# Optimization experiments

Hardware: AMD Instinct MI355X
Metric: run time of the kernel (lower is better)

Reference implementation:

```python
import jax, jax.numpy as jnp
import numpy as np

EPS = 1e-05
NEG = -1000000000.0

def rmsnorm(x):
    var = jnp.mean(x * x, axis=-1, keepdims=True)
    return x * jax.lax.rsqrt(var + EPS)

def apply_rotary(x, cos, sin):
    # x: [B,T,H,D], cos/sin: [T,D]
    d = x.shape[-1]
    x1, x2 = x[..., : d // 2], x[..., d // 2 :]
    half_rot = jnp.concatenate([-x2, x1], axis=-1)
    c = cos[None, :, None, :]
    s = sin[None, :, None, :]
    return x * c + half_rot * s

def setup_inputs() -> dict:
    key = jax.random.key(0)
    ks = jax.random.split(key, 12)
    B, T, C, H = 2, 2048, 1024, 16
    hd = C // H
    std = 0.02
    return {
        "x": jax.random.normal(ks[0], (B, T, C), jnp.float32),
        "x0": jax.random.normal(ks[1], (B, T, C), jnp.float32),
        "lambdaResid": jnp.ones((), jnp.float32),
        "lambdaX0": jnp.ones((), jnp.float32),
        "cos": jax.random.uniform(ks[2], (T, hd), jnp.float32),
        "sin": jax.random.uniform(ks[3], (T, hd), jnp.float32),
        "qWeight": jax.random.normal(ks[4], (C, C), jnp.float32) * std,
        "kWeight": jax.random.normal(ks[5], (C, C), jnp.float32) * std,
        "vWeight": jax.random.normal(ks[6], (C, C), jnp.float32) * std,
        "projWeight": jax.random.normal(ks[7], (C, C), jnp.float32) * std,
        "fcWeight": jax.random.normal(ks[8], (C, 4 * C), jnp.float32) * std,
        "mlpProjWeight": jax.random.normal(ks[9], (4 * C, C), jnp.float32) * std,
    }

def reference(x, x0, lambdaResid, lambdaX0, cos, sin,
              qWeight, kWeight, vWeight, projWeight, fcWeight, mlpProjWeight):
    B, T, C = x.shape
    hd = cos.shape[-1]
    H = C // hd
    scaled = x * lambdaResid + x0 * lambdaX0
    pre = rmsnorm(scaled)
    q = (pre @ qWeight).reshape(B, T, H, hd)
    k = (pre @ kWeight).reshape(B, T, H, hd)
    v = (pre @ vWeight).reshape(B, T, H, hd)
    q = rmsnorm(apply_rotary(q, cos, sin))  # [B,T,H,D]
    k = rmsnorm(apply_rotary(k, cos, sin))
    scores = jnp.einsum('bthd,bshd->bhts', q, k) / jnp.sqrt(jnp.float32(hd))
    mask = jnp.tril(jnp.ones((T, T), bool))
    scores = jnp.where(mask[None, None], scores, NEG)
    probs = jax.nn.softmax(scores, axis=-1)
    attn = jnp.einsum('bhts,bshd->bthd', probs, v).reshape(B, T, C)
    scaled = scaled + attn @ projWeight
    h = rmsnorm(scaled) @ fcWeight
    h = jnp.square(jax.nn.relu(h))
    return scaled + h @ mlpProjWeight
```

## Files before the change

### kernel.cpp

```cpp
#include <hip/hip_runtime.h>
#include <hip/hip_bf16.h>
#include <stdint.h>

typedef _Float16 f16;
typedef __attribute__((ext_vector_type(8))) _Float16 f16x8;
typedef __attribute__((ext_vector_type(4))) _Float16 f16x4;
typedef __attribute__((ext_vector_type(2))) __fp16 fp16x2;
typedef __attribute__((ext_vector_type(4))) float f32x4;

__device__ __forceinline__ void g2l16(const void* g, void* l) {
  __builtin_amdgcn_global_load_lds(
      (const __attribute__((address_space(1))) uint32_t*)g,
      (__attribute__((address_space(3))) uint32_t*)l, 16, 0, 0);
}

__device__ __forceinline__ uint32_t pkrtz(float a, float b) {
  union { fp16x2 h; uint32_t u; } z;
  z.h = __builtin_amdgcn_cvt_pkrtz(a, b);
  return z.u;
}

__global__ __launch_bounds__(256)
void wconv_all_kernel(const float* __restrict__ Wq, const float* __restrict__ Wk,
                      const float* __restrict__ Wv, const float* __restrict__ Wp,
                      const float* __restrict__ Wfc, const float* __restrict__ Wmp,
                      f16* __restrict__ Dq, f16* __restrict__ Dk, f16* __restrict__ Dv,
                      f16* __restrict__ Dp, f16* __restrict__ Dfc, f16* __restrict__ Dmp)
{
  __shared__ float tile[32][33];
  int id = blockIdx.x;
  const float* W; f16* Wt; int K, N, local;
  if      (id < 1024) { W = Wq;  Wt = Dq;  K = 1024; N = 1024; local = id; }
  else if (id < 2048) { W = Wk;  Wt = Dk;  K = 1024; N = 1024; local = id - 1024; }
  else if (id < 3072) { W = Wv;  Wt = Dv;  K = 1024; N = 1024; local = id - 2048; }
  else if (id < 4096) { W = Wp;  Wt = Dp;  K = 1024; N = 1024; local = id - 3072; }
  else if (id < 8192) { W = Wfc; Wt = Dfc; K = 1024; N = 4096; local = id - 4096; }
  else                { W = Wmp; Wt = Dmp; K = 4096; N = 1024; local = id - 8192; }
  int ntx = N >> 5;
  int n0 = (local % ntx) * 32, k0 = (local / ntx) * 32;
  int tx = threadIdx.x & 31, ty = threadIdx.x >> 5;
#pragma unroll
  for (int i = 0; i < 4; ++i)
    tile[ty + 8*i][tx] = W[(size_t)(k0 + ty + 8*i) * N + (n0 + tx)];
  __syncthreads();
#pragma unroll
  for (int i = 0; i < 4; ++i)
    Wt[(size_t)(n0 + ty + 8*i) * K + (k0 + tx)] = (f16)tile[tx][ty + 8*i];
}

__global__ __launch_bounds__(256)
void scale_rms_kernel(const float* __restrict__ x, const float* __restrict__ x0,
                      const float* __restrict__ lamR, const float* __restrict__ lamX,
                      float* __restrict__ scaled, f16* __restrict__ pre)
{
  const int C = 1024;
  int row = blockIdx.x, tid = threadIdx.x;
  float lr = lamR[0], lx = lamX[0];
  size_t base = (size_t)row * C;
  float4 xv = ((const float4*)(x + base))[tid];
  float4 zv = ((const float4*)(x0 + base))[tid];
  float4 sv;
  sv.x = xv.x*lr + zv.x*lx;  sv.y = xv.y*lr + zv.y*lx;
  sv.z = xv.z*lr + zv.z*lx;  sv.w = xv.w*lr + zv.w*lx;
  float ss = sv.x*sv.x + sv.y*sv.y + sv.z*sv.z + sv.w*sv.w;
#pragma unroll
  for (int off = 32; off >= 1; off >>= 1) ss += __shfl_xor(ss, off);
  __shared__ float red[4];
  if ((tid & 63) == 0) red[tid >> 6] = ss;
  __syncthreads();
  float tot = red[0] + red[1] + red[2] + red[3];
  float rs = rsqrtf(tot * (1.0f / 1024.0f) + 1e-5f);
  ((float4*)(scaled + base))[tid] = sv;
  f16* p = pre + base + tid * 4;
  p[0] = (f16)(sv.x * rs); p[1] = (f16)(sv.y * rs);
  p[2] = (f16)(sv.z * rs); p[3] = (f16)(sv.w * rs);
}

__global__ __launch_bounds__(256)
void combine_rms_kernel(const float* __restrict__ resid, const f16* __restrict__ p0,
                        const f16* __restrict__ p1, float* __restrict__ scaled2,
                        f16* __restrict__ pre2)
{
  const int C = 1024;
  int row = blockIdx.x, tid = threadIdx.x;
  size_t base = (size_t)row * C;
  float4 rv = ((const float4*)(resid + base))[tid];
  f16x4 av = ((const f16x4*)(p0 + base))[tid];
  f16x4 bv = ((const f16x4*)(p1 + base))[tid];
  float4 sv;
  sv.x = rv.x + (float)av[0] + (float)bv[0];
  sv.y = rv.y + (float)av[1] + (float)bv[1];
  sv.z = rv.z + (float)av[2] + (float)bv[2];
  sv.w = rv.w + (float)av[3] + (float)bv[3];
  float ss = sv.x*sv.x + sv.y*sv.y + sv.z*sv.z + sv.w*sv.w;
#pragma unroll
  for (int off = 32; off >= 1; off >>= 1) ss += __shfl_xor(ss, off);
  __shared__ float red[4];
  if ((tid & 63) == 0) red[tid >> 6] = ss;
  __syncthreads();
  float tot = red[0] + red[1] + red[2] + red[3];
  float rs = rsqrtf(tot * (1.0f / 1024.0f) + 1e-5f);
  ((float4*)(scaled2 + base))[tid] = sv;
  f16* p = pre2 + base + tid * 4;
  p[0] = (f16)(sv.x * rs); p[1] = (f16)(sv.y * rs);
  p[2] = (f16)(sv.z * rs); p[3] = (f16)(sv.w * rs);
}

__global__ __launch_bounds__(256)
void combine_out4_kernel(const float* __restrict__ resid, const f16* __restrict__ parts,
                         size_t pstride, float* __restrict__ out)
{
  size_t i = (size_t)blockIdx.x * 256 + threadIdx.x;
  float4 rv = ((const float4*)resid)[i];
  float4 sv = rv;
#pragma unroll
  for (int z = 0; z < 4; ++z) {
    f16x4 av = ((const f16x4*)(parts + z * pstride))[i];
    sv.x += (float)av[0]; sv.y += (float)av[1];
    sv.z += (float)av[2]; sv.w += (float)av[3];
  }
  ((float4*)out)[i] = sv;
}

__global__ __launch_bounds__(256)
void rope_rms_kernel(f16* __restrict__ Xq, f16* __restrict__ Xk,
                     const float* __restrict__ cs, const float* __restrict__ sn)
{
  const int MH = 4096 * 16;
  int ridx = blockIdx.x * 4 + (threadIdx.x >> 6);
  f16* X = (ridx < MH) ? Xq : Xk;
  if (ridx >= MH) ridx -= MH;
  int lane = threadIdx.x & 63;
  int h = ridx & 15;
  int bt = ridx >> 4;
  int t = bt & 2047;
  size_t base = (size_t)bt * 1024 + h * 64;
  float xv = (float)X[base + lane];
  float other = __shfl_xor(xv, 32);
  float rot = (lane < 32) ? -other : other;
  float c = cs[t * 64 + lane], s = sn[t * 64 + lane];
  float y = xv * c + rot * s;
  float ss = y * y;
#pragma unroll
  for (int off = 32; off >= 1; off >>= 1) ss += __shfl_xor(ss, off);
  float r = rsqrtf(ss * (1.0f / 64.0f) + 1e-5f);
  X[base + lane] = (f16)(y * r);
}

template<int EPI>
__global__ __launch_bounds__(256)
void gemm_kernel(const f16* __restrict__ A, const f16* __restrict__ Bt,
                 void* __restrict__ out, int M, int N, int K, int nb, int zb)
{
  __shared__ __align__(16) f16 smem[4 * 128 * 32];
  const int tid = threadIdx.x;
  const int wave = tid >> 6, lane = tid & 63;
  const int col = lane & 15, quad = lane >> 4;
  const int id = blockIdx.x;
  const int xcd = id & 7, s = id >> 3;
  const int n_i = s % nb;
  const int p = s / nb;
  const int mpx = (M >> 7) >> 3;
  const int zz = p / mpx;
  const int m_i = xcd * mpx + (p % mpx);
  const int m0 = m_i * 128, n0 = n_i * 128;
  const int wm = (wave >> 1) * 64, wn = (wave & 1) * 64;
  const int Ksub = K / zb;
  const int kBeg = zz * Ksub;
  const int nIter = Ksub >> 5;
  f32x4 acc[4][4] = {};

  const size_t rowb = (size_t)K * 2;
  const char* Agp = (const char*)A  + (size_t)m0 * rowb;
  const char* Bgp = (const char*)Bt + (size_t)n0 * rowb;

  const int r_st = (tid >> 2);
  const int cb_st = (tid & 3) << 4;
  const int lb0 = (wave * 64) << 4;
  const int lb1 = (256 + wave * 64) << 4;

#define STAGE(buf, k0)                                                           \
  {                                                                              \
    const size_t koff = (size_t)(k0) * 2;                                        \
    g2l16(Agp + (size_t)r_st * rowb + koff + cb_st,                              \
          (char*)smem + (buf) * 8192 + lb0);                                     \
    g2l16(Agp + (size_t)(r_st + 64) * rowb + koff + cb_st,                       \
          (char*)smem + (buf) * 8192 + lb1);                                     \
    g2l16(Bgp + (size_t)r_st * rowb + koff + cb_st,                              \
          (char*)smem + 16384 + (buf) * 8192 + lb0);                             \
    g2l16(Bgp + (size_t)(r_st + 64) * rowb + koff + cb_st,                       \
          (char*)smem + 16384 + (buf) * 8192 + lb1);                             \
  }

  STAGE(0, kBeg)
  for (int kt = 0; kt < nIter; ++kt) {
    __syncthreads();
    if (kt + 1 < nIter) STAGE((kt + 1) & 1, kBeg + (kt + 1) * 32)
    const f16* As = smem + (kt & 1) * 4096;
    const f16* Bs = smem + 8192 + (kt & 1) * 4096;
    f16x8 af[4], bf[4];
#pragma unroll
    for (int t = 0; t < 4; ++t)
      af[t] = *(const f16x8*)(As + (wm + t*16 + col) * 32 + quad * 8);
#pragma unroll
    for (int t = 0; t < 4; ++t)
      bf[t] = *(const f16x8*)(Bs + (wn + t*16 + col) * 32 + quad * 8);
#pragma unroll
    for (int mt = 0; mt < 4; ++mt)
#pragma unroll
      for (int nt = 0; nt < 4; ++nt)
        acc[mt][nt] = __builtin_amdgcn_mfma_f32_16x16x32_f16(af[mt], bf[nt], acc[mt][nt], 0, 0, 0);
  }
#undef STAGE
  f16* ep = smem + wave * 1024;
  f16* outz = (EPI == 4) ? ((f16*)out + (size_t)zz * M * N) : (f16*)out;
#pragma unroll
  for (int mt = 0; mt < 4; ++mt) {
#pragma unroll
    for (int nt = 0; nt < 4; ++nt) {
#pragma unroll
      for (int r = 0; r < 4; ++r) {
        float v = acc[mt][nt][r];
        if (EPI == 1) { float tv = v > 0.0f ? v : 0.0f; v = tv * tv; }
        ep[(quad * 4 + r) * 64 + ((nt ^ quad) * 16 + col)] = (f16)v;
      }
    }
#pragma unroll
    for (int j = 0; j < 2; ++j) {
      int e = j * 64 + lane;
      int row = e >> 3, rb = e & 7;
      int phys16 = (((rb >> 1) ^ (row >> 2)) << 1) + (rb & 1);
      f16x8 vv = *(const f16x8*)(ep + row * 64 + phys16 * 8);
      int grow = m0 + wm + mt * 16 + row;
      int gcol = n0 + wn + rb * 8;
      *(f16x8*)(outz + (size_t)grow * N + gcol) = vv;
    }
  }
}

__device__ __forceinline__ void stage256(const char* Agp, const char* Bgp, size_t rowb,
                                         char* lds, int st_r, size_t koff, int tid)
{
#pragma unroll
  for (int j = 0; j < 4; ++j) {
    g2l16(Agp + (size_t)(st_r + j * 64) * rowb + koff, lds + j * 8192 + tid * 16);
    g2l16(Bgp + (size_t)(st_r + j * 64) * rowb + koff, lds + 32768 + j * 8192 + tid * 16);
  }
}

template<int EPI>
__global__ __launch_bounds__(512, 2)
void gemm256_kernel(const f16* __restrict__ A, const f16* __restrict__ Bt,
                    void* __restrict__ out, int M, int N, int K, int nb, int zb)
{
  __shared__ __align__(16) f16 smem[65536];
  const int tid = threadIdx.x;
  const int wave = tid >> 6, lane = tid & 63;
  const int col = lane & 15, quad = lane >> 4;
  const int id = blockIdx.x;
  const int xcd = id & 7, sb = id >> 3;
  const int n_i = sb % nb;
  const int p = sb / nb;
  const int mpx = (M >> 8) >> 3;
  const int zz = p / mpx;
  const int m_i = xcd * mpx + (p % mpx);
  const int m0 = m_i * 256, n0 = n_i * 256;
  const int wm = (wave >> 2) * 128, wn = (wave & 3) * 64;
  const int Ksub = K / zb;
  const int kBeg = zz * Ksub;
  const int ntiles = Ksub >> 6;
  f32x4 acc[8][4] = {};

  const size_t rowb = (size_t)K * 2;
  const char* Agp = (const char*)A  + (size_t)m0 * rowb;
  const char* Bgp = (const char*)Bt + (size_t)n0 * rowb;

  const int st_r = tid >> 3;
  const size_t st_so = (size_t)(((tid & 7) ^ ((tid >> 3) & 7)) << 4);

  stage256(Agp, Bgp, rowb, (char*)smem,         st_r, (size_t)kBeg * 2 + st_so, tid);
  stage256(Agp, Bgp, rowb, (char*)smem + 65536, st_r, (size_t)(kBeg + 64) * 2 + st_so, tid);

  for (int t = 0; t < ntiles; ++t) {
    if (t < ntiles - 1) asm volatile("s_waitcnt vmcnt(8)" ::: "memory");
    else                asm volatile("s_waitcnt vmcnt(0)" ::: "memory");
    __builtin_amdgcn_s_barrier();
    asm volatile("" ::: "memory");

    const f16* As = smem + (t & 1) * 32768;
    const f16* Bs = As + 16384;
    f16x8 bf[4][2];
#pragma unroll
    for (int ct = 0; ct < 4; ++ct)
#pragma unroll
      for (int ks = 0; ks < 2; ++ks)
        bf[ct][ks] = *(const f16x8*)(Bs + (wn + ct*16 + col) * 64 +
                                     (((ks*4 + quad) ^ (col & 7)) << 3));
#pragma unroll
    for (int sp = 0; sp < 4; ++sp) {
      f16x8 af[2][2];
#pragma unroll
      for (int i = 0; i < 2; ++i)
#pragma unroll
        for (int ks = 0; ks < 2; ++ks)
          af[i][ks] = *(const f16x8*)(As + (wm + (sp*2 + i)*16 + col) * 64 +
                                      (((ks*4 + quad) ^ (col & 7)) << 3));
      __builtin_amdgcn_s_setprio(1);
#pragma unroll
      for (int i = 0; i < 2; ++i)
#pragma unroll
        for (int ct = 0; ct < 4; ++ct)
#pragma unroll
          for (int ks = 0; ks < 2; ++ks)
            acc[sp*2 + i][ct] = __builtin_amdgcn_mfma_f32_16x16x32_f16(
                af[i][ks], bf[ct][ks], acc[sp*2 + i][ct], 0, 0, 0);
      __builtin_amdgcn_s_setprio(0);
    }

    asm volatile("s_waitcnt lgkmcnt(0)" ::: "memory");
    __builtin_amdgcn_s_barrier();
    asm volatile("" ::: "memory");
    if (t + 2 < ntiles)
      stage256(Agp, Bgp, rowb, (char*)smem + (t & 1) * 65536, st_r,
               (size_t)(kBeg + (t + 2) * 64) * 2 + st_so, tid);
  }

  f16* ep = smem + wave * 1024;
  f16* outz = (EPI == 4) ? ((f16*)out + (size_t)zz * M * N) : (f16*)out;
#pragma unroll
  for (int mt = 0; mt < 8; ++mt) {
#pragma unroll
    for (int ct = 0; ct < 4; ++ct) {
#pragma unroll
      for (int r = 0; r < 4; ++r) {
        float v = acc[mt][ct][r];
        if (EPI == 1) { float tv = v > 0.0f ? v : 0.0f; v = tv * tv; }
        ep[(quad * 4 + r) * 64 + ((ct ^ quad) * 16 + col)] = (f16)v;
      }
    }
#pragma unroll
    for (int j = 0; j < 2; ++j) {
      int e = j * 64 + lane;
      int row = e >> 3, rb = e & 7;
      int phys16 = (((rb >> 1) ^ (row >> 2)) << 1) + (rb & 1);
      f16x8 vv = *(const f16x8*)(ep + row * 64 + phys16 * 8);
      int grow = m0 + wm + mt * 16 + row;
      int gcol = n0 + wn + rb * 8;
      *(f16x8*)(outz + (size_t)grow * N + gcol) = vv;
    }
  }
}

__global__ __launch_bounds__(512, 2)
void gemm256_qkv_kernel(const f16* __restrict__ A, const f16* __restrict__ Bt,
                        f16* __restrict__ qb, f16* __restrict__ kbuf, f16* __restrict__ vtg)
{
  const int K = 1024, nb = 12, ntiles = 16;
  __shared__ __align__(16) f16 smem[65536];
  const int tid = threadIdx.x;
  const int wave = tid >> 6, lane = tid & 63;
  const int col = lane & 15, quad = lane >> 4;
  const int id = blockIdx.x;
  const int xcd = id & 7, sb = id >> 3;
  const int n_i = sb % nb;
  const int m_i = xcd * 2 + (sb / nb);
  const int m0 = m_i * 256, n0 = n_i * 256;
  const int wm = (wave >> 2) * 128, wn = (wave & 3) * 64;
  f32x4 acc[8][4] = {};

  const size_t rowb = (size_t)K * 2;
  const char* Agp = (const char*)A  + (size_t)m0 * rowb;
  const char* Bgp = (const char*)Bt + (size_t)n0 * rowb;

  const int st_r = tid >> 3;
  const size_t st_so = (size_t)(((tid & 7) ^ ((tid >> 3) & 7)) << 4);

  stage256(Agp, Bgp, rowb, (char*)smem,         st_r, st_so, tid);
  stage256(Agp, Bgp, rowb, (char*)smem + 65536, st_r, (size_t)64 * 2 + st_so, tid);

  for (int t = 0; t < ntiles; ++t) {
    if (t < ntiles - 1) asm volatile("s_waitcnt vmcnt(8)" ::: "memory");
    else                asm volatile("s_waitcnt vmcnt(0)" ::: "memory");
    __builtin_amdgcn_s_barrier();
    asm volatile("" ::: "memory");

    const f16* As = smem + (t & 1) * 32768;
    const f16* Bs = As + 16384;
    f16x8 bf[4][2];
#pragma unroll
    for (int ct = 0; ct < 4; ++ct)
#pragma unroll
      for (int ks = 0; ks < 2; ++ks)
        bf[ct][ks] = *(const f16x8*)(Bs + (wn + ct*16 + col) * 64 +
                                     (((ks*4 + quad) ^ (col & 7)) << 3));
#pragma unroll
    for (int sp = 0; sp < 4; ++sp) {
      f16x8 af[2][2];
#pragma unroll
      for (int i = 0; i < 2; ++i)
#pragma unroll
        for (int ks = 0; ks < 2; ++ks)
          af[i][ks] = *(const f16x8*)(As + (wm + (sp*2 + i)*16 + col) * 64 +
                                      (((ks*4 + quad) ^ (col & 7)) << 3));
      __builtin_amdgcn_s_setprio(1);
#pragma unroll
      for (int i = 0; i < 2; ++i)
#pragma unroll
        for (int ct = 0; ct < 4; ++ct)
#pragma unroll
          for (int ks = 0; ks < 2; ++ks)
            acc[sp*2 + i][ct] = __builtin_amdgcn_mfma_f32_16x16x32_f16(
                af[i][ks], bf[ct][ks], acc[sp*2 + i][ct], 0, 0, 0);
      __builtin_amdgcn_s_setprio(0);
    }

    asm volatile("s_waitcnt lgkmcnt(0)" ::: "memory");
    __builtin_amdgcn_s_barrier();
    asm volatile("" ::: "memory");
    if (t + 2 < ntiles)
      stage256(Agp, Bgp, rowb, (char*)smem + (t & 1) * 65536, st_r,
               (size_t)((t + 2) * 64) * 2 + st_so, tid);
  }

  const int cw = n0 + wn;
  const int sel = cw >> 10;
  if (sel < 2) {
    f16* dst = (sel == 0) ? qb : kbuf;
    const int cbase = cw & 1023;
    f16* ep = smem + wave * 1024;
#pragma unroll
    for (int mt = 0; mt < 8; ++mt) {
#pragma unroll
      for (int ct = 0; ct < 4; ++ct)
#pragma unroll
        for (int r = 0; r < 4; ++r)
          ep[(quad * 4 + r) * 64 + ((ct ^ quad) * 16 + col)] = (f16)acc[mt][ct][r];
#pragma unroll
      for (int j = 0; j < 2; ++j) {
        int e = j * 64 + lane;
        int row = e >> 3, rb = e & 7;
        int phys16 = (((rb >> 1) ^ (row >> 2)) << 1) + (rb & 1);
        f16x8 vv = *(const f16x8*)(ep + row * 64 + phys16 * 8);
        int grow = m0 + wm + mt * 16 + row;
        *(f16x8*)(dst + (size_t)grow * 1024 + cbase + rb * 8) = vv;
      }
    }
  } else {
#pragma unroll
    for (int mt = 0; mt < 8; ++mt) {
      int t0 = m0 + wm + mt * 16 + quad * 4;
      int b = t0 >> 11, t = t0 & 2047;
#pragma unroll
      for (int ct = 0; ct < 4; ++ct) {
        int dd = (cw & 1023) + ct * 16 + col;
        int hh = dd >> 6, d = dd & 63;
        f16x4 vv;
#pragma unroll
        for (int r = 0; r < 4; ++r) vv[r] = (f16)acc[mt][ct][r];
        *(f16x4*)(vtg + ((size_t)((b * 16 + hh) * 64 + d)) * 2048 + t) = vv;
      }
    }
  }
}

__global__ __launch_bounds__(256, 5)
void attn_kernel(const f16* __restrict__ Q, const f16* __restrict__ Kc,
                 const f16* __restrict__ Vt, f16* __restrict__ O,
                 f16* __restrict__ pO, float* __restrict__ pL)
{
  const int T = 2048, C = 1024;
  __shared__ __align__(16) f16 Ks[2][64 * 64];
  __shared__ __align__(16) f16 Vs[2][64 * 64];
  const int tid = threadIdx.x, wave = tid >> 6, lane = tid & 63;
  const int col = lane & 15, quad = lane >> 4;
  const int bh = blockIdx.x, b = bh >> 4, h = bh & 15;

  const int u = blockIdx.y;
  int qt = 0, acc0 = 0, nc = 1;
  for (int q = 0; q < 32; ++q) {
    int c = (q + 8) >> 3;
    if (u < acc0 + c) { qt = q; nc = c; break; }
    acc0 += c;
  }
  const int ci = u - acc0;
  const int n = qt + 1;
  const int kt0 = (ci * n) / nc, kt1 = ((ci + 1) * n) / nc;
  const int q0 = qt * 64;

  const f16* qb = Q  + ((size_t)b * T) * C + h * 64;
  const f16* kb = Kc + ((size_t)b * T) * C + h * 64;
  const f16* vb = Vt + ((size_t)bh * 64) * T;

  f16x8 bq[2];
#pragma unroll
  for (int ks = 0; ks < 2; ++ks)
    bq[ks] = *(const f16x8*)(qb + (size_t)(q0 + wave*16 + col) * C + ks*32 + quad*8);

  f32x4 o_acc[4];
#pragma unroll
  for (int dt = 0; dt < 4; ++dt) o_acc[dt] = (f32x4){0.f,0.f,0.f,0.f};
  float l_acc = 0.f;

  const int srow = lane >> 3;
  const int sblk = (lane & 7) ^ srow;

#pragma unroll
  for (int i = 0; i < 2; ++i) {
    int r0 = wave * 16 + 8 * i;
    g2l16(kb + (size_t)(kt0 * 64 + r0 + srow) * C + sblk * 8, (char*)Ks[0] + r0 * 128);
    g2l16(vb + (size_t)(r0 + srow) * T + kt0 * 64 + sblk * 8, (char*)Vs[0] + r0 * 128);
  }

  const int cm = col & 7;
  const int c00 = quad,            c01 = 4 + (quad ^ 1);
  const int c10 = 8 + (quad ^ 2),  c11 = 12 + (quad ^ 3);
  const int o00 = (((c00 >> 1) ^ cm) << 3) + ((c00 & 1) << 2);
  const int o01 = (((c01 >> 1) ^ cm) << 3) + ((c01 & 1) << 2);
  const int o10 = (((c10 >> 1) ^ cm) << 3) + ((c10 & 1) << 2);
  const int o11 = (((c11 >> 1) ^ cm) << 3) + ((c11 & 1) << 2);

  int cur = 0;
  for (int kt = kt0; kt < kt1; ++kt) {
    __syncthreads();

    if (kt + 1 < kt1) {
      const int ks1 = (kt + 1) * 64;
#pragma unroll
      for (int i = 0; i < 2; ++i) {
        int r0 = wave * 16 + 8 * i;
        g2l16(kb + (size_t)(ks1 + r0 + srow) * C + sblk * 8, (char*)Ks[cur ^ 1] + r0 * 128);
        g2l16(vb + (size_t)(r0 + srow) * T + ks1 + sblk * 8, (char*)Vs[cur ^ 1] + r0 * 128);
      }
    }

    f32x4 s[4];
#pragma unroll
    for (int nt = 0; nt < 4; ++nt) s[nt] = (f32x4){0.f,0.f,0.f,0.f};
    __builtin_amdgcn_s_setprio(1);
#pragma unroll
    for (int ks = 0; ks < 2; ++ks) {
#pragma unroll
      for (int nt = 0; nt < 4; ++nt) {
        int key = nt * 16 + col;
        f16x8 ak = *(const f16x8*)(Ks[cur] + key * 64 + (((ks*4 + quad) ^ (key & 7)) * 8));
        s[nt] = __builtin_amdgcn_mfma_f32_16x16x32_f16(ak, bq[ks], s[nt], 0, 0, 0);
      }
    }
    __builtin_amdgcn_s_setprio(0);

    const bool masked = (kt == qt);
    const int qloc = wave * 16 + col;
    uint32_t pk[4][2];
    float l_tile = 0.f;
#pragma unroll
    for (int nt = 0; nt < 4; ++nt) {
      float p[4];
#pragma unroll
      for (int r = 0; r < 4; ++r) {
        float pv = __expf(s[nt][r] * 0.125f);
        if (masked && (nt * 16 + quad * 4 + r > qloc)) pv = 0.0f;
        p[r] = pv;
      }
      l_tile += (p[0] + p[1]) + (p[2] + p[3]);
      pk[nt][0] = pkrtz(p[0], p[1]);
      pk[nt][1] = pkrtz(p[2], p[3]);
    }
    l_acc += l_tile;

    union { uint32_t u[4]; f16x8 v; } pa0, pa1;
    pa0.u[0] = pk[0][0];
    pa0.u[1] = pk[0][1];
    pa0.u[2] = (uint32_t)__shfl_xor((int)pk[1][0], 16);
    pa0.u[3] = (uint32_t)__shfl_xor((int)pk[1][1], 16);
    pa1.u[0] = (uint32_t)__shfl_xor((int)pk[2][0], 32);
    pa1.u[1] = (uint32_t)__shfl_xor((int)pk[2][1], 32);
    pa1.u[2] = (uint32_t)__shfl_xor((int)pk[3][0], 48);
    pa1.u[3] = (uint32_t)__shfl_xor((int)pk[3][1], 48);

    __builtin_amdgcn_s_setprio(1);
#pragma unroll
    for (int dt = 0; dt < 4; ++dt) {
      const f16* vrow = Vs[cur] + (dt * 16 + col) * 64;
      union { struct { f16x4 lo, hi; } p; f16x8 v; } bv0, bv1;
      bv0.p.lo = *(const f16x4*)(vrow + o00);
      bv0.p.hi = *(const f16x4*)(vrow + o01);
      bv1.p.lo = *(const f16x4*)(vrow + o10);
      bv1.p.hi = *(const f16x4*)(vrow + o11);
      o_acc[dt] = __builtin_amdgcn_mfma_f32_16x16x32_f16(pa0.v, bv0.v, o_acc[dt], 0, 0, 0);
      o_acc[dt] = __builtin_amdgcn_mfma_f32_16x16x32_f16(pa1.v, bv1.v, o_acc[dt], 0, 0, 0);
    }
    __builtin_amdgcn_s_setprio(0);
    cur ^= 1;
  }

  l_acc += __shfl_xor(l_acc, 16);
  l_acc += __shfl_xor(l_acc, 32);

  if (nc == 1) {
    float linv[4];
#pragma unroll
    for (int r = 0; r < 4; ++r)
      linv[r] = 1.0f / __shfl(l_acc, quad * 4 + r);
#pragma unroll
    for (int dt = 0; dt < 4; ++dt) {
#pragma unroll
      for (int r = 0; r < 4; ++r) {
        int qr = q0 + wave * 16 + quad * 4 + r;
        float v = o_acc[dt][r] * linv[r];
        O[((size_t)b * T + qr) * C + h * 64 + dt * 16 + col] = (f16)v;
      }
    }
  } else {
    const size_t slot = (size_t)bh * 80 + u;
    f16* po = pO + slot * 4096;
#pragma unroll
    for (int dt = 0; dt < 4; ++dt)
#pragma unroll
      for (int r = 0; r < 4; ++r)
        po[(wave * 16 + quad * 4 + r) * 64 + dt * 16 + col] = (f16)o_acc[dt][r];
    if (quad == 0) pL[slot * 64 + wave * 16 + col] = l_acc;
  }
}

__global__ __launch_bounds__(256)
void attn_combine_kernel(const f16* __restrict__ pO, const float* __restrict__ pL,
                         f16* __restrict__ O)
{
  const int T = 2048, C = 1024;
  const int bh = blockIdx.x, b = bh >> 4, h = bh & 15;
  const int qt = 8 + blockIdx.y;
  const int nc = (qt + 8) >> 3;
  int pre = 0;
  for (int q = 0; q < qt; ++q) pre += (q + 8) >> 3;
  const size_t slot0 = (size_t)bh * 80 + pre;

  const int t = threadIdx.x;
  const int row = t >> 2, dq = (t & 3) * 16;

  float L = 0.f;
  for (int ci = 0; ci < nc; ++ci) L += pL[(slot0 + ci) * 64 + row];
  const float inv = 1.0f / L;

  float acc[16] = {};
  for (int ci = 0; ci < nc; ++ci) {
    const f16x8* p = (const f16x8*)(pO + (slot0 + ci) * 4096 + row * 64 + dq);
    f16x8 v0 = p[0], v1 = p[1];
#pragma unroll
    for (int j = 0; j < 8; ++j) { acc[j] += (float)v0[j]; acc[8 + j] += (float)v1[j]; }
  }
  f16x8 o0, o1;
#pragma unroll
  for (int j = 0; j < 8; ++j) { o0[j] = (f16)(acc[j] * inv); o1[j] = (f16)(acc[8 + j] * inv); }
  f16* dst = O + ((size_t)b * T + qt * 64 + row) * C + h * 64 + dq;
  ((f16x8*)dst)[0] = o0;
  ((f16x8*)dst)[1] = o1;
}

extern "C" void kernel_launch(void* const* d_in, const int* in_sizes, int n_in,
                              void* d_out, int out_size, void* d_ws, size_t ws_size,
                              hipStream_t stream)
{
  const float* x    = (const float*)d_in[0];
  const float* x0   = (const float*)d_in[1];
  const float* lamR = (const float*)d_in[2];
  const float* lamX = (const float*)d_in[3];
  const float* cs   = (const float*)d_in[4];
  const float* sn   = (const float*)d_in[5];
  const float* Wq   = (const float*)d_in[6];
  const float* Wk   = (const float*)d_in[7];
  const float* Wv   = (const float*)d_in[8];
  const float* Wp   = (const float*)d_in[9];
  const float* Wfc  = (const float*)d_in[10];
  const float* Wmp  = (const float*)d_in[11];
  float* out = (float*)d_out;

  const int B = 2, T = 2048, C = 1024, H = 16;
  const int M = B * T;
  const size_t MB = 1ull << 20;
  char* ws = (char*)d_ws;
  f16*   Wqkv_t = (f16*)(ws + 0 * MB);
  f16*   Wp_t   = (f16*)(ws + 6 * MB);
  f16*   Wfc_t  = (f16*)(ws + 8 * MB);
  f16*   Wmp_t  = (f16*)(ws + 16 * MB);
  float* scaled  = (float*)(ws + 24 * MB);
  f16*   pre     = (f16*)(ws + 40 * MB);
  f16*   qb      = (f16*)(ws + 48 * MB);
  f16*   kbuf    = (f16*)(ws + 56 * MB);
  f16*   vtg     = (f16*)(ws + 64 * MB);
  float* scaled2 = (float*)(ws + 72 * MB);
  f16*   hbuf    = (f16*)(ws + 88 * MB);
  f16*   attnOut = pre;
  f16*   pre2    = qb;
  f16*   projP   = (f16*)(ws + 88 * MB);
  f16*   mlpP    = (f16*)(ws + 24 * MB);
  f16*   attnPO  = (f16*)(ws + 88 * MB);
  float* attnPL  = (float*)(ws + 108 * MB);

  dim3 tb(256);
  dim3 tb5(512);
  wconv_all_kernel<<<dim3(12288), tb, 0, stream>>>(
      Wq, Wk, Wv, Wp, Wfc, Wmp,
      Wqkv_t, Wqkv_t + 1024*1024, Wqkv_t + 2048*1024, Wp_t, Wfc_t, Wmp_t);

  scale_rms_kernel<<<M, tb, 0, stream>>>(x, x0, lamR, lamX, scaled, pre);

  gemm256_qkv_kernel<<<dim3(192), tb5, 0, stream>>>(pre, Wqkv_t, qb, kbuf, vtg);

  rope_rms_kernel<<<(M * H) / 2, tb, 0, stream>>>(qb, kbuf, cs, sn);

  attn_kernel<<<dim3(B * H, 80), tb, 0, stream>>>(qb, kbuf, vtg, attnOut, attnPO, attnPL);
  attn_combine_kernel<<<dim3(B * H, 24), tb, 0, stream>>>(attnPO, attnPL, attnOut);

  gemm_kernel<4><<<dim3(8 * 32 * 2), tb, 0, stream>>>(attnOut, Wp_t, projP, M, C, C, 8, 2);
  combine_rms_kernel<<<M, tb, 0, stream>>>(scaled, projP, projP + (size_t)M*C, scaled2, pre2);

  gemm256_kernel<1><<<dim3(256), tb5, 0, stream>>>(pre2, Wfc_t, hbuf, M, 4*C, C, 16, 1);

  gemm256_kernel<4><<<dim3(256), tb5, 0, stream>>>(hbuf, Wmp_t, mlpP, M, C, 4*C, 4, 4);
  combine_out4_kernel<<<(M*C)/1024, tb, 0, stream>>>(scaled2, mlpP, (size_t)M*C, out);
}
```

Before: 351.8 us.

## Prefetch K/V two tiles ahead with partial vmcnt waits in attention

The attention loop now issues the async global-to-LDS loads for tile kt+2 right after tile kt is consumed, and starts with two tiles in flight. At the top of each iteration it waits only until the current tile's loads land (vmcnt(4)) rather than draining all loads with a full __syncthreads. This deepens the load pipeline so memory latency overlaps more of the MFMA work. It adds a second barrier per iteration and relies on exact hand-counted vmcnt values, which break if the compiler emits other vector-memory ops in the loop.

```diff
diff --git a/kernel.cpp b/kernel.cpp
--- a/kernel.cpp
+++ b/kernel.cpp
@@ -504,12 +504,21 @@
   const int srow = lane >> 3;
   const int sblk = (lane & 7) ^ srow;
 
-#pragma unroll
-  for (int i = 0; i < 2; ++i) {
-    int r0 = wave * 16 + 8 * i;
-    g2l16(kb + (size_t)(kt0 * 64 + r0 + srow) * C + sblk * 8, (char*)Ks[0] + r0 * 128);
-    g2l16(vb + (size_t)(r0 + srow) * T + kt0 * 64 + sblk * 8, (char*)Vs[0] + r0 * 128);
-  }
+#define STAGEKV(ktile, bi)                                                       \
+  {                                                                              \
+    const int kk = (ktile) * 64;                                                 \
+    _Pragma("unroll")                                                            \
+    for (int i = 0; i < 2; ++i) {                                                \
+      int r0 = wave * 16 + 8 * i;                                                \
+      g2l16(kb + (size_t)(kk + r0 + srow) * C + sblk * 8,                        \
+            (char*)Ks[bi] + r0 * 128);                                           \
+      g2l16(vb + (size_t)(r0 + srow) * T + kk + sblk * 8,                        \
+            (char*)Vs[bi] + r0 * 128);                                           \
+    }                                                                            \
+  }
+
+  STAGEKV(kt0, 0)
+  if (kt0 + 1 < kt1) STAGEKV(kt0 + 1, 1)
 
   const int cm = col & 7;
   const int c00 = quad,            c01 = 4 + (quad ^ 1);
@@ -521,17 +530,10 @@
 
   int cur = 0;
   for (int kt = kt0; kt < kt1; ++kt) {
-    __syncthreads();
-
-    if (kt + 1 < kt1) {
-      const int ks1 = (kt + 1) * 64;
-#pragma unroll
-      for (int i = 0; i < 2; ++i) {
-        int r0 = wave * 16 + 8 * i;
-        g2l16(kb + (size_t)(ks1 + r0 + srow) * C + sblk * 8, (char*)Ks[cur ^ 1] + r0 * 128);
-        g2l16(vb + (size_t)(r0 + srow) * T + ks1 + sblk * 8, (char*)Vs[cur ^ 1] + r0 * 128);
-      }
-    }
+    if (kt + 1 < kt1) asm volatile("s_waitcnt vmcnt(4)" ::: "memory");
+    else              asm volatile("s_waitcnt vmcnt(0)" ::: "memory");
+    __builtin_amdgcn_s_barrier();
+    asm volatile("" ::: "memory");
 
     f32x4 s[4];
 #pragma unroll
@@ -590,8 +592,14 @@
       o_acc[dt] = __builtin_amdgcn_mfma_f32_16x16x32_f16(pa1.v, bv1.v, o_acc[dt], 0, 0, 0);
     }
     __builtin_amdgcn_s_setprio(0);
+
+    asm volatile("s_waitcnt lgkmcnt(0)" ::: "memory");
+    __builtin_amdgcn_s_barrier();
+    asm volatile("" ::: "memory");
+    if (kt + 2 < kt1) STAGEKV(kt + 2, cur)
     cur ^= 1;
   }
+#undef STAGEKV
 
   l_acc += __shfl_xor(l_acc, 16);
   l_acc += __shfl_xor(l_acc, 32);
```

Result: no change. 357.3 us (+1.6%).
